# Kernel tuning notes

Hardware: AMD Instinct MI355X
Metric: run time of the kernel (lower is better)

Reference implementation:

```python
import jax, jax.numpy as jnp
import numpy as np

H = 16  # attention heads


def setup_inputs() -> dict:
    key = jax.random.key(0)
    k0, k1, k2 = jax.random.split(key, 3)
    B, T, C = 2, 2048, 1024
    x = jax.random.normal(k0, (B, T, C), dtype=jnp.float32)
    W_attn = jax.random.normal(k1, (3 * C, C), dtype=jnp.float32) * 0.02
    W_proj = jax.random.normal(k2, (C, C), dtype=jnp.float32) * 0.02
    b_proj = jnp.zeros((C,), dtype=jnp.float32)
    return {"x": x, "W_attn": W_attn, "W_proj": W_proj, "b_proj": b_proj}


def reference(x, W_attn, W_proj, b_proj):
    # Eval-mode (dropout = identity), rotational_embeddings=False, flash=False path.
    B, T, C = x.shape
    d = C // H
    qkv = jnp.einsum('btc,fc->btf', x, W_attn)          # [B,T,3C] fused QKV proj
    q, k, v = jnp.split(qkv, 3, axis=-1)
    # [B,T,C] -> [B,H,T,d]
    q = q.reshape(B, T, H, d).transpose(0, 2, 1, 3)
    k = k.reshape(B, T, H, d).transpose(0, 2, 1, 3)
    v = v.reshape(B, T, H, d).transpose(0, 2, 1, 3)
    scale = 1.0 / np.sqrt(d).astype(np.float32)
    att = jnp.einsum('bhqd,bhkd->bhqk', q, k) * scale    # full TxT scores (no mask)
    att = jax.nn.softmax(att, axis=-1)
    y = jnp.einsum('bhqk,bhkd->bhqd', att, v)            # [B,H,T,d]
    y = y.transpose(0, 2, 1, 3).reshape(B, T, C)
    return jnp.einsum('btc,oc->bto', y, W_proj) + b_proj
```

## Files before the change

kernel.cpp:

```cpp
#include <hip/hip_runtime.h>
#include <hip/hip_bf16.h>
#include <stdint.h>

typedef __attribute__((ext_vector_type(8))) short bf16x8;
typedef __attribute__((ext_vector_type(4))) float f32x4;
typedef __attribute__((ext_vector_type(4))) unsigned u32x4;

#define MFMA16(A,B,C) __builtin_amdgcn_mfma_f32_16x16x32_bf16(A,B,C,0,0,0)


__device__ inline void gld_lds16(const __hip_bfloat16* g, __hip_bfloat16* l) {
  __builtin_amdgcn_global_load_lds(
      (const __attribute__((address_space(1))) void*)g,
      (__attribute__((address_space(3))) void*)l, 16, 0, 0);
}

__device__ inline unsigned pkbf(float a, float b) {
  __hip_bfloat162 t = __float22bfloat162_rn(float2{a, b});
  return *(unsigned*)&t;
}

__device__ inline void quad_mix(unsigned &a, unsigned &b) {
#if __has_builtin(__builtin_amdgcn_permlane32_swap) && __has_builtin(__builtin_amdgcn_permlane16_swap)
  auto r1 = __builtin_amdgcn_permlane32_swap(a, b, false, false);
  auto r2 = __builtin_amdgcn_permlane16_swap(r1[0], r1[1], false, false);
  a = r2[0];
  b = r2[1];
#else
  int lane = (int)(threadIdx.x & 63);
  int g = lane >> 4;
  int lm = lane & 15;
  int slo = (((g << 1) & 3) << 4) | lm;
  int shi = ((((g << 1) | 1) & 3) << 4) | lm;
  unsigned t0 = (unsigned)__shfl((int)a, slo, 64);
  unsigned t1 = (unsigned)__shfl((int)b, slo, 64);
  unsigned t2 = (unsigned)__shfl((int)a, shi, 64);
  unsigned t3 = (unsigned)__shfl((int)b, shi, 64);
  bool hi = g >= 2;
  unsigned na = hi ? t1 : t0;
  unsigned nb = hi ? t3 : t2;
  a = na;
  b = nb;
#endif
}

__global__ __launch_bounds__(256)
void cvt_bf16(const float* __restrict__ s0, __hip_bfloat16* __restrict__ d0, int n0,
              const float* __restrict__ s1, __hip_bfloat16* __restrict__ d1, int n1,
              const float* __restrict__ s2, __hip_bfloat16* __restrict__ d2, int n2)
{
  const float* s; __hip_bfloat16* d; int n;
  if      (blockIdx.y == 0) { s = s0; d = d0; n = n0; }
  else if (blockIdx.y == 1) { s = s1; d = d1; n = n1; }
  else                      { s = s2; d = d2; n = n2; }
  int idx = (blockIdx.x * 256 + threadIdx.x) * 8;
  if (idx >= n) return;
  float4 u0 = *(const float4*)(s + idx);
  float4 u1 = *(const float4*)(s + idx + 4);
  __hip_bfloat16 t[8];
  t[0] = __float2bfloat16(u0.x); t[1] = __float2bfloat16(u0.y);
  t[2] = __float2bfloat16(u0.z); t[3] = __float2bfloat16(u0.w);
  t[4] = __float2bfloat16(u1.x); t[5] = __float2bfloat16(u1.y);
  t[6] = __float2bfloat16(u1.z); t[7] = __float2bfloat16(u1.w);
  *(int4*)(d + idx) = *(const int4*)t;
}

template<int BM, int BN, typename TC>
__global__ __launch_bounds__(256)
void gemm_bt(const __hip_bfloat16* __restrict__ A,
             const __hip_bfloat16* __restrict__ B,
             TC* __restrict__ C,
             const float* __restrict__ bias,
             __hip_bfloat16* __restrict__ vtg,
             int M, int N, int K)
{
  constexpr int MI = BM / 32;
  constexpr int NJ = BN / 32;
  constexpr int NP = (BM + BN) / 64;

  __shared__ __align__(16) __hip_bfloat16 As[BM * 32];
  __shared__ __align__(16) __hip_bfloat16 Bs[BN * 32];

  const int tid  = threadIdx.x;
  const int lane = tid & 63;
  const int w    = tid >> 6;
  const int lm   = lane & 15;
  const int g    = lane >> 4;

  const int bm = blockIdx.y * BM;
  const int bn = blockIdx.x * BN;
  const int rm = (w >> 1) * (BM / 2);
  const int cn = (w & 1) * (BN / 2);

  const f32x4 fzero = {0.0f, 0.0f, 0.0f, 0.0f};
  f32x4 acc[MI][NJ];
  for (int i = 0; i < MI; i++)
    for (int j = 0; j < NJ; j++)
      acc[i][j] = fzero;

  for (int k0 = 0; k0 < K; k0 += 32) {
    __syncthreads();
#pragma unroll
    for (int p = 0; p < NP; p++) {
      int c = tid + p * 256;
      if (c < BM * 4)
        gld_lds16(&A[(size_t)(bm + (c >> 2)) * K + k0 + (c & 3) * 8], &As[c * 8]);
      else {
        int cb = c - BM * 4;
        gld_lds16(&B[(size_t)(bn + (cb >> 2)) * K + k0 + (cb & 3) * 8], &Bs[cb * 8]);
      }
    }
    __syncthreads();

    bf16x8 af[MI], bfr[NJ];
#pragma unroll
    for (int i = 0; i < MI; i++)
      af[i] = *(const bf16x8*)&As[(rm + 16 * i + lm) * 32 + 8 * g];
#pragma unroll
    for (int j = 0; j < NJ; j++)
      bfr[j] = *(const bf16x8*)&Bs[(cn + 16 * j + lm) * 32 + 8 * g];
#pragma unroll
    for (int i = 0; i < MI; i++)
#pragma unroll
      for (int j = 0; j < NJ; j++)
        acc[i][j] = MFMA16(af[i], bfr[j], acc[i][j]);
  }

  if (vtg != nullptr && bn >= 2048) {
#pragma unroll
    for (int j = 0; j < NJ; j++) {
      int colv = bn + cn + 16 * j + lm - 2048;
      int vh = colv >> 6, dd = colv & 63;
#pragma unroll
      for (int i = 0; i < MI; i++) {
        int m0 = bm + rm + 16 * i + 4 * g;
        int bb = m0 >> 11, t0 = m0 & 2047;
        __hip_bfloat16 t4[4];
#pragma unroll
        for (int r = 0; r < 4; r++) t4[r] = __float2bfloat16(acc[i][j][r]);
        *(int2*)&vtg[((size_t)(bb * 16 + vh) * 64 + dd) * 2048 + t0] =
            *(const int2*)t4;
      }
    }
    return;
  }

  const float qs = (vtg != nullptr && bn < 1024) ? (0.125f * 1.4426950408889634f)
                                                 : 1.0f;
#pragma unroll
  for (int j = 0; j < NJ; j++) {
    int coln = bn + cn + 16 * j + lm;
    float bv = bias ? bias[coln] : 0.0f;
#pragma unroll
    for (int i = 0; i < MI; i++) {
#pragma unroll
      for (int r = 0; r < 4; r++) {
        int rowm = bm + rm + 16 * i + 4 * g + r;
        float v = acc[i][j][r] * qs + bv;
        if constexpr (sizeof(TC) == 2)
          C[(size_t)rowm * N + coln] = __float2bfloat16(v);
        else
          C[(size_t)rowm * N + coln] = v;
      }
    }
  }
}

__global__ __launch_bounds__(256)
void mha(const __hip_bfloat16* __restrict__ qkv,
         const __hip_bfloat16* __restrict__ vtg,
         __hip_bfloat16* __restrict__ yout,
         __hip_bfloat16* __restrict__ po,
         float* __restrict__ pl,
         int nsteps)
{
  const int T = 2048, F = 3072, Cc = 1024;
  const int bh = blockIdx.x;
  const int b  = bh >> 4, h = bh & 15;
  const int qb0 = blockIdx.y * 128;
  const int z   = blockIdx.z;
  const int kvb = z * 32 * nsteps;

  const int tid  = threadIdx.x;
  const int lane = tid & 63;
  const int w    = tid >> 6;
  const int lm   = lane & 15;
  const int g    = lane >> 4;

  __shared__ __align__(16) __hip_bfloat16 Ks[2][32 * 64];
  __shared__ __align__(16) __hip_bfloat16 Vs[2][64 * 32];

  const size_t rowbase = (size_t)b * T * F;
  const int hoff = h * 64;
  const __hip_bfloat16* Kbase = qkv + rowbase + 1024 + hoff;
  const __hip_bfloat16* Vtb   = vtg + (size_t)(b * 16 + h) * 64 * 2048;

  const int qw = qb0 + 32 * w;
  bf16x8 aq[2][2];
#pragma unroll
  for (int mt = 0; mt < 2; mt++)
#pragma unroll
    for (int e = 0; e < 2; e++)
      aq[mt][e] = *(const bf16x8*)
          &qkv[rowbase + (size_t)(qw + 16 * mt + lm) * F + hoff + 32 * e + 8 * g];

  const f32x4 fzero = {0.0f, 0.0f, 0.0f, 0.0f};
  f32x4 yacc[2][4];
  float lsum[2] = {0.0f, 0.0f};
#pragma unroll
  for (int mt = 0; mt < 2; mt++)
#pragma unroll
    for (int c = 0; c < 4; c++) yacc[mt][c] = fzero;

  const int r0  = tid >> 3;
  const int swK = (tid & 7) ^ (r0 & 7);
  const int vdd = tid >> 2;
  const int vk  = (tid & 3) ^ ((tid >> 3) & 3);
  const int sxK = lm & 7;
  const int sxV = (lm >> 1) & 3;

  gld_lds16(Kbase + (size_t)(kvb + r0) * F + swK * 8, &Ks[0][tid * 8]);
  gld_lds16(Vtb + (size_t)vdd * 2048 + kvb + vk * 8, &Vs[0][tid * 8]);

  for (int t = 0; t < nsteps; t++) {
    const int buf = t & 1;
    __syncthreads();
    if (t + 1 < nsteps) {
      const int kvn = kvb + (t + 1) * 32;
      gld_lds16(Kbase + (size_t)(kvn + r0) * F + swK * 8, &Ks[buf ^ 1][tid * 8]);
      gld_lds16(Vtb + (size_t)vdd * 2048 + kvn + vk * 8, &Vs[buf ^ 1][tid * 8]);
    }

    bf16x8 kf[2][2];
#pragma unroll
    for (int c2 = 0; c2 < 2; c2++) {
      kf[c2][0] = *(const bf16x8*)&Ks[buf][(16 * c2 + lm) * 64 + ((0 + g) ^ sxK) * 8];
      kf[c2][1] = *(const bf16x8*)&Ks[buf][(16 * c2 + lm) * 64 + ((4 + g) ^ sxK) * 8];
    }
#pragma unroll
    for (int mt = 0; mt < 2; mt++) {
      f32x4 st[2];
#pragma unroll
      for (int c2 = 0; c2 < 2; c2++) {
        st[c2] = MFMA16(kf[c2][0], aq[mt][0], fzero);
        st[c2] = MFMA16(kf[c2][1], aq[mt][1], st[c2]);
      }

      unsigned pkv[2][2];
#pragma unroll
      for (int c2 = 0; c2 < 2; c2++)
#pragma unroll
        for (int u = 0; u < 2; u++) {
          float p0 = __builtin_amdgcn_exp2f(st[c2][2 * u]);
          float p1 = __builtin_amdgcn_exp2f(st[c2][2 * u + 1]);
          lsum[mt] += p0 + p1;
          pkv[c2][u] = pkbf(p0, p1);
        }

      unsigned f0 = pkv[0][0], f2 = pkv[1][0];
      quad_mix(f0, f2);
      unsigned f1 = pkv[0][1], f3 = pkv[1][1];
      quad_mix(f1, f3);
      u32x4 fv = {f0, f1, f2, f3};
      bf16x8 ap = __builtin_bit_cast(bf16x8, fv);

#pragma unroll
      for (int c = 0; c < 4; c++) {
        bf16x8 bv = *(const bf16x8*)&Vs[buf][(16 * c + lm) * 32 + (g ^ sxV) * 8];
        yacc[mt][c] = MFMA16(ap, bv, yacc[mt][c]);
      }
    }
  }

  float lred[2];
#pragma unroll
  for (int mt = 0; mt < 2; mt++) {
    float ls = lsum[mt];
    ls += __shfl_xor(ls, 16);
    ls += __shfl_xor(ls, 32);
    lred[mt] = ls;
  }

#pragma unroll
  for (int mt = 0; mt < 2; mt++) {
    if (yout != nullptr) {
      float rv[4];
#pragma unroll
      for (int r = 0; r < 4; r++)
        rv[r] = 1.0f / __shfl(lred[mt], 4 * g + r, 64);
#pragma unroll
      for (int c = 0; c < 4; c++)
#pragma unroll
        for (int r = 0; r < 4; r++) {
          int qrow = qw + 16 * mt + 4 * g + r;
          yout[(size_t)(b * T + qrow) * Cc + hoff + 16 * c + lm] =
              __float2bfloat16(yacc[mt][c][r] * rv[r]);
        }
    } else {
      __hip_bfloat16* pz = po + (size_t)z * 4096 * 1024;
      float* plz = pl + (size_t)z * 4096 * 16;
#pragma unroll
      for (int c = 0; c < 4; c++)
#pragma unroll
        for (int r = 0; r < 4; r++) {
          int qrow = qw + 16 * mt + 4 * g + r;
          pz[(size_t)(b * T + qrow) * Cc + hoff + 16 * c + lm] =
              __float2bfloat16(yacc[mt][c][r]);
        }
      if (lane < 16)
        plz[(b * T + qw + 16 * mt + lane) * 16 + h] = lred[mt];
    }
  }
}

__global__ __launch_bounds__(256)
void combine(const __hip_bfloat16* __restrict__ po,
             const float* __restrict__ pl,
             __hip_bfloat16* __restrict__ y)
{
  int idx = (blockIdx.x * 256 + threadIdx.x) * 8;
  int row = idx >> 10, c = idx & 1023, h = c >> 6;
  float la = pl[row * 16 + h];
  float lb = pl[4096 * 16 + row * 16 + h];
  float rinv = 1.0f / (la + lb);
  const __hip_bfloat16* pa = po + idx;
  const __hip_bfloat16* pb = po + 4096 * 1024 + idx;
  __hip_bfloat16 t[8];
#pragma unroll
  for (int j = 0; j < 8; j++)
    t[j] = __float2bfloat16(
        (__bfloat162float(pa[j]) + __bfloat162float(pb[j])) * rinv);
  *(int4*)(y + idx) = *(const int4*)t;
}

extern "C" void kernel_launch(void* const* d_in, const int* in_sizes, int n_in,
                              void* d_out, int out_size, void* d_ws, size_t ws_size,
                              hipStream_t stream)
{
  const float* x  = (const float*)d_in[0];
  const float* Wa = (const float*)d_in[1];
  const float* Wp = (const float*)d_in[2];
  const float* bp = (const float*)d_in[3];
  float* out = (float*)d_out;

  const int BT = 4096, C = 1024, F3 = 3072;
  char* ws = (char*)d_ws;
  __hip_bfloat16* qkv  = (__hip_bfloat16*)ws;
  __hip_bfloat16* vtg  = (__hip_bfloat16*)(ws + 25165824);
  __hip_bfloat16* xbf  = (__hip_bfloat16*)(ws + 33554432);
  __hip_bfloat16* yb   = xbf;
  __hip_bfloat16* Wabf = (__hip_bfloat16*)(ws + 41943040);
  __hip_bfloat16* Wpbf = (__hip_bfloat16*)(ws + 48234496);
  __hip_bfloat16* Opar = (__hip_bfloat16*)(ws + 50331648);
  float*          lpar = (float*)(ws + 67108864);
  const size_t need_split = 67633152;

  cvt_bf16<<<dim3(2048, 3), 256, 0, stream>>>(
      x, xbf, BT * C, Wa, Wabf, F3 * C, Wp, Wpbf, C * C);
  gemm_bt<128, 128, __hip_bfloat16>
      <<<dim3(F3 / 128, BT / 128), 256, 0, stream>>>(xbf, Wabf, qkv, nullptr, vtg,
                                                     BT, F3, C);
  if (ws_size >= need_split) {
    mha<<<dim3(32, 16, 2), 256, 0, stream>>>(qkv, vtg, nullptr, Opar, lpar, 32);
    combine<<<dim3(BT * C / 2048), 256, 0, stream>>>(Opar, lpar, yb);
  } else {
    mha<<<dim3(32, 16, 1), 256, 0, stream>>>(qkv, vtg, yb, nullptr, nullptr, 64);
  }
  gemm_bt<64, 128, float>
      <<<dim3(C / 128, BT / 64), 256, 0, stream>>>(yb, Wpbf, out, bp, nullptr,
                                                   BT, C, C);
}
```

Before: 206.1 us.

## Split attention KV into four chunks, batch PV MFMAs, raise mha occupancy

The KV split-K of the attention kernel goes from 2 to 4 chunks when the workspace is large enough, so the grid has twice as many blocks, and the combine kernel becomes templated on the chunk count. The PV MFMAs for both query tiles now run after both softmax tiles are ready, sharing each V fragment load, and MFMA sections are wrapped in s_setprio. launch_bounds adds a minimum of 8 blocks per CU. The trade-off is more partial-output traffic in combine, possible register pressure from the occupancy bound, and a dependence on the workspace size.

```diff
diff --git a/kernel.cpp b/kernel.cpp
--- a/kernel.cpp
+++ b/kernel.cpp
@@ -166,7 +166,7 @@
   }
 }
 
-__global__ __launch_bounds__(256)
+__global__ __launch_bounds__(256, 8)
 void mha(const __hip_bfloat16* __restrict__ qkv,
          const __hip_bfloat16* __restrict__ vtg,
          __hip_bfloat16* __restrict__ yout,
@@ -237,14 +237,18 @@
       kf[c2][0] = *(const bf16x8*)&Ks[buf][(16 * c2 + lm) * 64 + ((0 + g) ^ sxK) * 8];
       kf[c2][1] = *(const bf16x8*)&Ks[buf][(16 * c2 + lm) * 64 + ((4 + g) ^ sxK) * 8];
     }
+
+    bf16x8 ap[2];
 #pragma unroll
     for (int mt = 0; mt < 2; mt++) {
       f32x4 st[2];
+      __builtin_amdgcn_s_setprio(1);
 #pragma unroll
       for (int c2 = 0; c2 < 2; c2++) {
         st[c2] = MFMA16(kf[c2][0], aq[mt][0], fzero);
         st[c2] = MFMA16(kf[c2][1], aq[mt][1], st[c2]);
       }
+      __builtin_amdgcn_s_setprio(0);
 
       unsigned pkv[2][2];
 #pragma unroll
@@ -262,14 +266,17 @@
       unsigned f1 = pkv[0][1], f3 = pkv[1][1];
       quad_mix(f1, f3);
       u32x4 fv = {f0, f1, f2, f3};
-      bf16x8 ap = __builtin_bit_cast(bf16x8, fv);
-
-#pragma unroll
-      for (int c = 0; c < 4; c++) {
-        bf16x8 bv = *(const bf16x8*)&Vs[buf][(16 * c + lm) * 32 + (g ^ sxV) * 8];
-        yacc[mt][c] = MFMA16(ap, bv, yacc[mt][c]);
-      }
-    }
+      ap[mt] = __builtin_bit_cast(bf16x8, fv);
+    }
+
+    __builtin_amdgcn_s_setprio(1);
+#pragma unroll
+    for (int c = 0; c < 4; c++) {
+      bf16x8 bv = *(const bf16x8*)&Vs[buf][(16 * c + lm) * 32 + (g ^ sxV) * 8];
+      yacc[0][c] = MFMA16(ap[0], bv, yacc[0][c]);
+      yacc[1][c] = MFMA16(ap[1], bv, yacc[1][c]);
+    }
+    __builtin_amdgcn_s_setprio(0);
   }
 
   float lred[2];
@@ -313,6 +320,7 @@
   }
 }
 
+template<int Z>
 __global__ __launch_bounds__(256)
 void combine(const __hip_bfloat16* __restrict__ po,
              const float* __restrict__ pl,
@@ -320,16 +328,22 @@
 {
   int idx = (blockIdx.x * 256 + threadIdx.x) * 8;
   int row = idx >> 10, c = idx & 1023, h = c >> 6;
-  float la = pl[row * 16 + h];
-  float lb = pl[4096 * 16 + row * 16 + h];
-  float rinv = 1.0f / (la + lb);
-  const __hip_bfloat16* pa = po + idx;
-  const __hip_bfloat16* pb = po + 4096 * 1024 + idx;
+  float l = 0.0f;
+#pragma unroll
+  for (int zi = 0; zi < Z; zi++)
+    l += pl[zi * 4096 * 16 + row * 16 + h];
+  float rinv = 1.0f / l;
+  float acc[8] = {0.f, 0.f, 0.f, 0.f, 0.f, 0.f, 0.f, 0.f};
+#pragma unroll
+  for (int zi = 0; zi < Z; zi++) {
+    int4 raw = *(const int4*)(po + (size_t)zi * 4096 * 1024 + idx);
+    const __hip_bfloat16* pa = (const __hip_bfloat16*)&raw;
+#pragma unroll
+    for (int j = 0; j < 8; j++) acc[j] += __bfloat162float(pa[j]);
+  }
   __hip_bfloat16 t[8];
 #pragma unroll
-  for (int j = 0; j < 8; j++)
-    t[j] = __float2bfloat16(
-        (__bfloat162float(pa[j]) + __bfloat162float(pb[j])) * rinv);
+  for (int j = 0; j < 8; j++) t[j] = __float2bfloat16(acc[j] * rinv);
   *(int4*)(y + idx) = *(const int4*)t;
 }
 
@@ -352,17 +366,22 @@
   __hip_bfloat16* Wabf = (__hip_bfloat16*)(ws + 41943040);
   __hip_bfloat16* Wpbf = (__hip_bfloat16*)(ws + 48234496);
   __hip_bfloat16* Opar = (__hip_bfloat16*)(ws + 50331648);
-  float*          lpar = (float*)(ws + 67108864);
-  const size_t need_split = 67633152;
+  float*          lpar = (float*)(ws + 83886080);
+  float*          lpar2 = (float*)(ws + 67108864);
+  const size_t need4 = 84934656;
+  const size_t need2 = 67633152;
 
   cvt_bf16<<<dim3(2048, 3), 256, 0, stream>>>(
       x, xbf, BT * C, Wa, Wabf, F3 * C, Wp, Wpbf, C * C);
   gemm_bt<128, 128, __hip_bfloat16>
       <<<dim3(F3 / 128, BT / 128), 256, 0, stream>>>(xbf, Wabf, qkv, nullptr, vtg,
                                                      BT, F3, C);
-  if (ws_size >= need_split) {
-    mha<<<dim3(32, 16, 2), 256, 0, stream>>>(qkv, vtg, nullptr, Opar, lpar, 32);
-    combine<<<dim3(BT * C / 2048), 256, 0, stream>>>(Opar, lpar, yb);
+  if (ws_size >= need4) {
+    mha<<<dim3(32, 16, 4), 256, 0, stream>>>(qkv, vtg, nullptr, Opar, lpar, 16);
+    combine<4><<<dim3(BT * C / 2048), 256, 0, stream>>>(Opar, lpar, yb);
+  } else if (ws_size >= need2) {
+    mha<<<dim3(32, 16, 2), 256, 0, stream>>>(qkv, vtg, nullptr, Opar, lpar2, 32);
+    combine<2><<<dim3(BT * C / 2048), 256, 0, stream>>>(Opar, lpar2, yb);
   } else {
     mha<<<dim3(32, 16, 1), 256, 0, stream>>>(qkv, vtg, yb, nullptr, nullptr, 64);
   }
```

Result: slower. 400.7 us (+94.4%).
